# Kernel optimization log

Hardware: AMD Instinct MI355X
Metric: run time of the kernel (lower is better)

Reference implementation:

```python
import jax, jax.numpy as jnp
import numpy as np

B, S, H = 32, 1024, 1024

def setup_inputs() -> dict:
    key = jax.random.key(0)
    k1, k2, k3, k4, k5 = jax.random.split(key, 5)
    scale = 1.0 / np.sqrt(H)
    return {
        "decoder_hidden": jax.random.normal(k1, (B, H), jnp.float32),
        "encoder_outputs": jax.random.normal(k2, (B, S, H), jnp.float32),
        "U_w": jax.random.normal(k3, (H, H), jnp.float32) * scale,
        "W_w": jax.random.normal(k4, (H, H), jnp.float32) * scale,
        "v_w": jax.random.normal(k5, (H,), jnp.float32) * scale,
    }

def reference(decoder_hidden, encoder_outputs, U_w, W_w, v_w):
    # U(decoder_hidden): [B, H] @ [H, H]^T -> [B, H], broadcast over S
    U_h = jnp.einsum('bh,oh->bo', decoder_hidden, U_w)          # [B, H]
    W_s = jnp.einsum('bsh,oh->bso', encoder_outputs, W_w)       # [B, S, H]
    # v(tanh(U_h + W_s)) -> attention scores [B, S]
    att = jnp.einsum('bsh,h->bs', jnp.tanh(U_h[:, None, :] + W_s), v_w)
    alpha = jax.nn.softmax(att, axis=1)                          # [B, S]
    context = jnp.einsum('bs,bsh->bh', alpha, encoder_outputs)   # [B, H]
    return (context, alpha)
```

## Files before the change

### kernel.cpp

```cpp
#include <hip/hip_runtime.h>
#include <hip/hip_bf16.h>
#include <cstdint>
#include <cstddef>

#define B_DIM 32
#define S_DIM 1024
#define H_DIM 1024
#define M_DIM (B_DIM * S_DIM)

typedef __attribute__((ext_vector_type(8))) short bf16x8;
typedef __attribute__((ext_vector_type(4))) float f32x4;

static __device__ __forceinline__ unsigned short f2bf(float f) {
  unsigned u = __float_as_uint(f);
  u = (u + 0x7FFFu + ((u >> 16) & 1u)) >> 16;
  return (unsigned short)u;
}
static __device__ __forceinline__ float bf2f(unsigned short u) {
  return __uint_as_float(((unsigned)u) << 16);
}
static __device__ __forceinline__ float fast_tanh(float x) {
  return 1.f - 2.f / (__expf(2.f * x) + 1.f);
}

static __device__ __forceinline__ void gload16(const unsigned short* g, char* l) {
  __builtin_amdgcn_global_load_lds(
      (const __attribute__((address_space(1))) unsigned int*)g,
      (__attribute__((address_space(3))) unsigned int*)l, 16, 0, 0);
}

__global__ void k_prep_all(const float* __restrict__ E, unsigned short* __restrict__ Eb,
                           const float* __restrict__ W, unsigned short* __restrict__ Wb,
                           const float* __restrict__ dh, const float* __restrict__ Uw,
                           float* __restrict__ Uh) {
  const int bid = blockIdx.x;
  if (bid < 2048) {
    const int n8 = M_DIM * (H_DIM / 8);
    const int stride = 2048 * 256;
    for (int idx = bid * 256 + threadIdx.x; idx < n8; idx += stride) {
      const float4* gp = (const float4*)(E + (size_t)idx * 8);
      float4 lo = gp[0], hi = gp[1];
      bf16x8 w;
      w[0] = (short)f2bf(lo.x); w[1] = (short)f2bf(lo.y);
      w[2] = (short)f2bf(lo.z); w[3] = (short)f2bf(lo.w);
      w[4] = (short)f2bf(hi.x); w[5] = (short)f2bf(hi.y);
      w[6] = (short)f2bf(hi.z); w[7] = (short)f2bf(hi.w);
      *(bf16x8*)(Eb + (size_t)idx * 8) = w;
    }
  } else if (bid < 3072) {
    const int idx = (bid - 2048) * 256 + threadIdx.x;
    float4 v = ((const float4*)W)[idx];
    ushort4 o;
    o.x = f2bf(v.x); o.y = f2bf(v.y); o.z = f2bf(v.z); o.w = f2bf(v.w);
    ((ushort4*)Wb)[idx] = o;
  } else {
    const int wave = threadIdx.x >> 6;
    const int lane = threadIdx.x & 63;
    const int o = (bid - 3072) * 4 + wave;
    float uw[16];
#pragma unroll
    for (int k = 0; k < 16; ++k) uw[k] = Uw[o * H_DIM + k * 64 + lane];
    for (int b = 0; b < B_DIM; ++b) {
      float acc = 0.f;
#pragma unroll
      for (int k = 0; k < 16; ++k) acc += uw[k] * dh[b * H_DIM + k * 64 + lane];
#pragma unroll
      for (int msk = 32; msk >= 1; msk >>= 1) acc += __shfl_xor(acc, msk, 64);
      if (lane == 0) Uh[b * H_DIM + o] = acc;
    }
  }
}

#define A3_BM 128
#define A3_BN 256
#define A3_BUF 49152
#define NT_FAST 4

__launch_bounds__(512, 2)
__global__ void k_att4(const unsigned short* __restrict__ Eb,
                       const unsigned short* __restrict__ Wb,
                       const float* __restrict__ Uh,
                       const float* __restrict__ vw,
                       float* __restrict__ att_p) {
  __shared__ __align__(16) char lds[3 * A3_BUF];

  const int bid = blockIdx.x;
  const int xj = bid & 7;
  const int q  = bid >> 3;
  const int n_tile = q & 3;
  const int m_tile = ((q >> 2) << 3) | xj;
  const int m0 = m_tile * A3_BM;
  const int n0 = n_tile * A3_BN;
  const int b  = m0 >> 10;

  const int tid  = threadIdx.x;
  const int wid  = tid >> 6;
  const int lane = tid & 63;
  const int wm = (wid >> 2) * 64;
  const int wn = (wid & 3) * 64;

  size_t offA[2]; int ldsA[2];
  size_t offB[4]; int ldsB[4];
#pragma unroll
  for (int j = 0; j < 2; ++j) {
    const int chunk = j * 512 + tid;
    const int r  = chunk >> 3;
    const int c8 = (chunk & 7) ^ (r & 7);
    offA[j] = (size_t)(m0 + r) * H_DIM + c8 * 8;
    ldsA[j] = j * 8192 + wid * 1024;
  }
#pragma unroll
  for (int j = 0; j < 4; ++j) {
    const int chunk = j * 512 + tid;
    const int r  = chunk >> 3;
    const int c8 = (chunk & 7) ^ (r & 7);
    offB[j] = (size_t)(n0 + r) * H_DIM + c8 * 8;
    ldsB[j] = 16384 + j * 8192 + wid * 1024;
  }

  auto stage_all = [&](int t) {
    char* dst = lds + (t % 3) * A3_BUF;
    const size_t k0 = (size_t)t * 64;
#pragma unroll
    for (int j = 0; j < 2; ++j) gload16(Eb + offA[j] + k0, dst + ldsA[j]);
#pragma unroll
    for (int j = 0; j < 4; ++j) gload16(Wb + offB[j] + k0, dst + ldsB[j]);
  };

  const int fr_row = lane & 15;
  const int fr_k8  = lane >> 4;

  f32x4 acc[4][4];
#pragma unroll
  for (int mf = 0; mf < 4; ++mf)
#pragma unroll
    for (int nf = 0; nf < 4; ++nf) acc[mf][nf] = (f32x4)(0.0f);

  stage_all(0);
  stage_all(1);

  for (int t = 0; t < 16; ++t) {
    if (t < 15) asm volatile("s_waitcnt vmcnt(6)" ::: "memory");
    else        asm volatile("s_waitcnt vmcnt(0)" ::: "memory");
    __builtin_amdgcn_s_barrier();

    const char* As = lds + (t % 3) * A3_BUF;
    const char* Bs = As + 16384;
    char* dst = lds + ((t + 2) % 3) * A3_BUF;
    const size_t k2 = (size_t)(t + 2) * 64;
    const bool doStage = (t <= 13);

#pragma unroll
    for (int kh = 0; kh < 2; ++kh) {
      const int kb = kh * 32 + fr_k8 * 8;
      bf16x8 af[4], bfr[4];
#pragma unroll
      for (int mf = 0; mf < 4; ++mf) {
        const int row = wm + mf * 16 + fr_row;
        const int addr = (row * 128 + kb * 2) ^ ((row & 7) << 4);
        af[mf] = *(const bf16x8*)(As + addr);
      }
#pragma unroll
      for (int nf = 0; nf < 4; ++nf) {
        const int row = wn + nf * 16 + fr_row;
        const int addr = (row * 128 + kb * 2) ^ ((row & 7) << 4);
        bfr[nf] = *(const bf16x8*)(Bs + addr);
      }
      if (doStage) {
        if (kh == 0) {
          gload16(Eb + offA[0] + k2, dst + ldsA[0]);
          gload16(Eb + offA[1] + k2, dst + ldsA[1]);
          gload16(Wb + offB[0] + k2, dst + ldsB[0]);
        } else {
          gload16(Wb + offB[1] + k2, dst + ldsB[1]);
          gload16(Wb + offB[2] + k2, dst + ldsB[2]);
          gload16(Wb + offB[3] + k2, dst + ldsB[3]);
        }
      }
      __builtin_amdgcn_s_barrier();
      __builtin_amdgcn_s_setprio(1);
#pragma unroll
      for (int mf = 0; mf < 4; ++mf)
#pragma unroll
        for (int nf = 0; nf < 4; ++nf)
          acc[mf][nf] = __builtin_amdgcn_mfma_f32_16x16x32_bf16(af[mf], bfr[nf], acc[mf][nf], 0, 0, 0);
      __builtin_amdgcn_s_setprio(0);
      __builtin_amdgcn_s_barrier();
    }
  }

  float* red = (float*)lds;

  const int col = lane & 15;
  const int rhi = lane >> 4;
  float uh[4], vv[4];
#pragma unroll
  for (int nf = 0; nf < 4; ++nf) {
    const int o = n0 + wn + nf * 16 + col;
    uh[nf] = Uh[b * H_DIM + o];
    vv[nf] = vw[o];
  }
#pragma unroll
  for (int mf = 0; mf < 4; ++mf) {
    float rs[4];
#pragma unroll
    for (int jj = 0; jj < 4; ++jj) {
      float s = 0.f;
#pragma unroll
      for (int nf = 0; nf < 4; ++nf) {
        const float x = acc[mf][nf][jj] + uh[nf];
        s += fast_tanh(x) * vv[nf];
      }
      rs[jj] = s;
    }
#pragma unroll
    for (int msk = 1; msk < 16; msk <<= 1) {
#pragma unroll
      for (int jj = 0; jj < 4; ++jj) rs[jj] += __shfl_xor(rs[jj], msk, 64);
    }
    if (col == 0) {
#pragma unroll
      for (int jj = 0; jj < 4; ++jj) {
        const int local = mf * 16 + rhi * 4 + jj;
        red[wid * 64 + local] = rs[jj];
      }
    }
  }
  __syncthreads();
  if (tid < 128) {
    const int h4 = (tid >> 6) * 4;
    const int loc = tid & 63;
    float sum = 0.f;
#pragma unroll
    for (int j = 0; j < 4; ++j) sum += red[(h4 + j) * 64 + loc];
    att_p[(size_t)n_tile * M_DIM + m0 + tid] = sum;
  }
}

__global__ void k_ctx_sm(const unsigned short* __restrict__ Eb,
                         const float* __restrict__ att_p,
                         float* __restrict__ alpha_out,
                         float* __restrict__ ctx_p) {
  const int bid = blockIdx.x;
  const int b  = bid >> 2;
  const int sq = bid & 3;
  const int tid = threadIdx.x;
  __shared__ float red[8];
  __shared__ float qa[256];

  float a[4];
  float mx = -1e30f;
#pragma unroll
  for (int i = 0; i < 4; ++i) {
    const int s = i * 256 + tid;
    float v = 0.f;
#pragma unroll
    for (int t = 0; t < NT_FAST; ++t) v += att_p[(size_t)t * M_DIM + b * S_DIM + s];
    a[i] = v;
    mx = fmaxf(mx, v);
  }
#pragma unroll
  for (int msk = 32; msk >= 1; msk >>= 1) mx = fmaxf(mx, __shfl_xor(mx, msk, 64));
  if ((tid & 63) == 0) red[tid >> 6] = mx;
  __syncthreads();
  mx = fmaxf(fmaxf(red[0], red[1]), fmaxf(red[2], red[3]));
  float sum = 0.f;
#pragma unroll
  for (int i = 0; i < 4; ++i) { a[i] = __expf(a[i] - mx); sum += a[i]; }
#pragma unroll
  for (int msk = 32; msk >= 1; msk >>= 1) sum += __shfl_xor(sum, msk, 64);
  if ((tid & 63) == 0) red[4 + (tid >> 6)] = sum;
  __syncthreads();
  const float inv = 1.f / (red[4] + red[5] + red[6] + red[7]);
  if (sq == 0) {
#pragma unroll
    for (int i = 0; i < 4; ++i) alpha_out[b * S_DIM + i * 256 + tid] = a[i] * inv;
  }
  qa[tid] = a[sq] * inv;
  __syncthreads();

  const int h = tid * 4;
  const unsigned short* ep = Eb + (size_t)b * S_DIM * H_DIM + (size_t)(sq * 256) * H_DIM + h;
  float4 acc = make_float4(0.f, 0.f, 0.f, 0.f);
  for (int s = 0; s < 256; ++s) {
    const float al = qa[s];
    ushort4 v = *(const ushort4*)(ep + (size_t)s * H_DIM);
    acc.x += al * bf2f(v.x);
    acc.y += al * bf2f(v.y);
    acc.z += al * bf2f(v.z);
    acc.w += al * bf2f(v.w);
  }
  *(float4*)&ctx_p[(size_t)sq * (B_DIM * H_DIM) + b * H_DIM + h] = acc;
}

__global__ void k_ctx_reduce(const float* __restrict__ ctx_p, float* __restrict__ ctx) {
  const int i = blockIdx.x * 256 + threadIdx.x;
  ctx[i] = ctx_p[i] + ctx_p[32768 + i] + ctx_p[65536 + i] + ctx_p[98304 + i];
}

extern "C" void kernel_launch(void* const* d_in, const int* in_sizes, int n_in,
                              void* d_out, int out_size, void* d_ws, size_t ws_size,
                              hipStream_t stream) {
  (void)in_sizes; (void)n_in; (void)out_size; (void)ws_size;
  const float* dh  = (const float*)d_in[0];
  const float* enc = (const float*)d_in[1];
  const float* Uw  = (const float*)d_in[2];
  const float* Ww  = (const float*)d_in[3];
  const float* vw  = (const float*)d_in[4];
  float* ctx_out = (float*)d_out;
  float* alpha   = (float*)d_out + M_DIM;

  char* ws = (char*)d_ws;
  const size_t EB_BYTES = (size_t)M_DIM * H_DIM * 2;

  unsigned short* Eb = (unsigned short*)ws;
  unsigned short* Wb = (unsigned short*)(ws + EB_BYTES);
  float* Uh    = (float*)(ws + EB_BYTES + (2u << 20));
  float* att_p = (float*)(ws + EB_BYTES + (2u << 20) + (128u << 10));
  float* ctx_p = (float*)(ws + EB_BYTES + (2u << 20) + (128u << 10) + (1u << 20));

  k_prep_all<<<3328, 256, 0, stream>>>(enc, Eb, Ww, Wb, dh, Uw, Uh);
  k_att4<<<1024, 512, 0, stream>>>(Eb, Wb, Uh, vw, att_p);
  k_ctx_sm<<<128, 256, 0, stream>>>(Eb, att_p, alpha, ctx_p);
  k_ctx_reduce<<<128, 256, 0, stream>>>(ctx_p, ctx_out);
}
```

Measured before the change: 151.5 us.

## Enlarge attention GEMM tile to 256x256 with double-buffered LDS staging

Doubles the M tile of the attention-score GEMM from 128 to 256 rows, so each wave computes a 128x64 sub-tile with 8x4 MFMA accumulators. The grid drops from 1024 to 512 blocks. The LDS pipeline changes from a 3-stage ring with loads spread across the kh sub-steps to a 2-stage double buffer, where the next K slice is issued at the top of each iteration. The goal is higher arithmetic intensity and less global/LDS traffic per FLOP, at the cost of 128 KB of LDS per block, much higher register pressure (possible spills under launch_bounds(512,2)), and shallower prefetch.

```diff
diff --git a/kernel.cpp b/kernel.cpp
--- a/kernel.cpp
+++ b/kernel.cpp
@@ -71,58 +71,52 @@
   }
 }
 
-#define A3_BM 128
-#define A3_BN 256
-#define A3_BUF 49152
+#define A5_BM 256
+#define A5_BN 256
+#define A5_BUF 65536
 #define NT_FAST 4
 
 __launch_bounds__(512, 2)
-__global__ void k_att4(const unsigned short* __restrict__ Eb,
+__global__ void k_att5(const unsigned short* __restrict__ Eb,
                        const unsigned short* __restrict__ Wb,
                        const float* __restrict__ Uh,
                        const float* __restrict__ vw,
                        float* __restrict__ att_p) {
-  __shared__ __align__(16) char lds[3 * A3_BUF];
+  __shared__ __align__(16) char lds[2 * A5_BUF];
 
   const int bid = blockIdx.x;
   const int xj = bid & 7;
   const int q  = bid >> 3;
   const int n_tile = q & 3;
   const int m_tile = ((q >> 2) << 3) | xj;
-  const int m0 = m_tile * A3_BM;
-  const int n0 = n_tile * A3_BN;
+  const int m0 = m_tile * A5_BM;
+  const int n0 = n_tile * A5_BN;
   const int b  = m0 >> 10;
 
   const int tid  = threadIdx.x;
   const int wid  = tid >> 6;
   const int lane = tid & 63;
-  const int wm = (wid >> 2) * 64;
+  const int wm = (wid >> 2) * 128;
   const int wn = (wid & 3) * 64;
 
-  size_t offA[2]; int ldsA[2];
-  size_t offB[4]; int ldsB[4];
-#pragma unroll
-  for (int j = 0; j < 2; ++j) {
+  size_t offA[4], offB[4];
+  int ldsA[4], ldsB[4];
+#pragma unroll
+  for (int j = 0; j < 4; ++j) {
     const int chunk = j * 512 + tid;
     const int r  = chunk >> 3;
     const int c8 = (chunk & 7) ^ (r & 7);
     offA[j] = (size_t)(m0 + r) * H_DIM + c8 * 8;
+    offB[j] = (size_t)(n0 + r) * H_DIM + c8 * 8;
     ldsA[j] = j * 8192 + wid * 1024;
-  }
-#pragma unroll
-  for (int j = 0; j < 4; ++j) {
-    const int chunk = j * 512 + tid;
-    const int r  = chunk >> 3;
-    const int c8 = (chunk & 7) ^ (r & 7);
-    offB[j] = (size_t)(n0 + r) * H_DIM + c8 * 8;
-    ldsB[j] = 16384 + j * 8192 + wid * 1024;
-  }
-
-  auto stage_all = [&](int t) {
-    char* dst = lds + (t % 3) * A3_BUF;
+    ldsB[j] = 32768 + j * 8192 + wid * 1024;
+  }
+
+  auto stage = [&](int t) {
+    char* dst = lds + (t & 1) * A5_BUF;
     const size_t k0 = (size_t)t * 64;
 #pragma unroll
-    for (int j = 0; j < 2; ++j) gload16(Eb + offA[j] + k0, dst + ldsA[j]);
+    for (int j = 0; j < 4; ++j) gload16(Eb + offA[j] + k0, dst + ldsA[j]);
 #pragma unroll
     for (int j = 0; j < 4; ++j) gload16(Wb + offB[j] + k0, dst + ldsB[j]);
   };
@@ -130,32 +124,31 @@
   const int fr_row = lane & 15;
   const int fr_k8  = lane >> 4;
 
-  f32x4 acc[4][4];
-#pragma unroll
-  for (int mf = 0; mf < 4; ++mf)
+  f32x4 acc[8][4];
+#pragma unroll
+  for (int mf = 0; mf < 8; ++mf)
 #pragma unroll
     for (int nf = 0; nf < 4; ++nf) acc[mf][nf] = (f32x4)(0.0f);
 
-  stage_all(0);
-  stage_all(1);
+  stage(0);
 
   for (int t = 0; t < 16; ++t) {
-    if (t < 15) asm volatile("s_waitcnt vmcnt(6)" ::: "memory");
-    else        asm volatile("s_waitcnt vmcnt(0)" ::: "memory");
+    if (t < 15) {
+      stage(t + 1);
+      asm volatile("s_waitcnt vmcnt(8)" ::: "memory");
+    } else {
+      asm volatile("s_waitcnt vmcnt(0)" ::: "memory");
+    }
     __builtin_amdgcn_s_barrier();
 
-    const char* As = lds + (t % 3) * A3_BUF;
-    const char* Bs = As + 16384;
-    char* dst = lds + ((t + 2) % 3) * A3_BUF;
-    const size_t k2 = (size_t)(t + 2) * 64;
-    const bool doStage = (t <= 13);
-
+    const char* As = lds + (t & 1) * A5_BUF;
+    const char* Bs = As + 32768;
 #pragma unroll
     for (int kh = 0; kh < 2; ++kh) {
       const int kb = kh * 32 + fr_k8 * 8;
-      bf16x8 af[4], bfr[4];
-#pragma unroll
-      for (int mf = 0; mf < 4; ++mf) {
+      bf16x8 af[8], bfr[4];
+#pragma unroll
+      for (int mf = 0; mf < 8; ++mf) {
         const int row = wm + mf * 16 + fr_row;
         const int addr = (row * 128 + kb * 2) ^ ((row & 7) << 4);
         af[mf] = *(const bf16x8*)(As + addr);
@@ -166,21 +159,10 @@
         const int addr = (row * 128 + kb * 2) ^ ((row & 7) << 4);
         bfr[nf] = *(const bf16x8*)(Bs + addr);
       }
-      if (doStage) {
-        if (kh == 0) {
-          gload16(Eb + offA[0] + k2, dst + ldsA[0]);
-          gload16(Eb + offA[1] + k2, dst + ldsA[1]);
-          gload16(Wb + offB[0] + k2, dst + ldsB[0]);
-        } else {
-          gload16(Wb + offB[1] + k2, dst + ldsB[1]);
-          gload16(Wb + offB[2] + k2, dst + ldsB[2]);
-          gload16(Wb + offB[3] + k2, dst + ldsB[3]);
-        }
-      }
       __builtin_amdgcn_s_barrier();
       __builtin_amdgcn_s_setprio(1);
 #pragma unroll
-      for (int mf = 0; mf < 4; ++mf)
+      for (int mf = 0; mf < 8; ++mf)
 #pragma unroll
         for (int nf = 0; nf < 4; ++nf)
           acc[mf][nf] = __builtin_amdgcn_mfma_f32_16x16x32_bf16(af[mf], bfr[nf], acc[mf][nf], 0, 0, 0);
@@ -201,7 +183,7 @@
     vv[nf] = vw[o];
   }
 #pragma unroll
-  for (int mf = 0; mf < 4; ++mf) {
+  for (int mf = 0; mf < 8; ++mf) {
     float rs[4];
 #pragma unroll
     for (int jj = 0; jj < 4; ++jj) {
@@ -222,17 +204,17 @@
 #pragma unroll
       for (int jj = 0; jj < 4; ++jj) {
         const int local = mf * 16 + rhi * 4 + jj;
-        red[wid * 64 + local] = rs[jj];
+        red[wid * 128 + local] = rs[jj];
       }
     }
   }
   __syncthreads();
-  if (tid < 128) {
-    const int h4 = (tid >> 6) * 4;
-    const int loc = tid & 63;
+  if (tid < 256) {
+    const int mhalf = tid >> 7;
+    const int loc = tid & 127;
     float sum = 0.f;
 #pragma unroll
-    for (int j = 0; j < 4; ++j) sum += red[(h4 + j) * 64 + loc];
+    for (int j = 0; j < 4; ++j) sum += red[(mhalf * 4 + j) * 128 + loc];
     att_p[(size_t)n_tile * M_DIM + m0 + tid] = sum;
   }
 }
@@ -320,7 +302,7 @@
   float* ctx_p = (float*)(ws + EB_BYTES + (2u << 20) + (128u << 10) + (1u << 20));
 
   k_prep_all<<<3328, 256, 0, stream>>>(enc, Eb, Ww, Wb, dh, Uw, Uh);
-  k_att4<<<1024, 512, 0, stream>>>(Eb, Wb, Uh, vw, att_p);
+  k_att5<<<512, 512, 0, stream>>>(Eb, Wb, Uh, vw, att_p);
   k_ctx_sm<<<128, 256, 0, stream>>>(Eb, att_p, alpha, ctx_p);
   k_ctx_reduce<<<128, 256, 0, stream>>>(ctx_p, ctx_out);
 }
```

New measurement: 148.6 us. About the same (-1.9%).
